# Optimization experiments

Measured on AMD Instinct MI355X. Metric: run time of the kernel, lower is better.

## Reference

```python
import jax, jax.numpy as jnp
import numpy as np

B, IN_UNITS, IN_CHANNELS, NUM_UNITS, UNIT_SIZE = 128, 32, 4096, 10, 16
NUM_ITER = 3


def setup_inputs() -> dict:
    key = jax.random.key(0)
    k1, k2 = jax.random.split(key)
    # x: primary-capsule output [B, in_units, in_channels]
    x = jax.random.normal(k1, (B, IN_UNITS, IN_CHANNELS), dtype=jnp.float32)
    # W: routing weights, torch param shape [1, C, J, D, K] with batch dim dropped
    W = jax.random.normal(k2, (IN_CHANNELS, NUM_UNITS, UNIT_SIZE, IN_UNITS), dtype=jnp.float32)
    return {"x": x, "W": W}


def reference(x, W):
    b_sz = x.shape[0]
    C, J = W.shape[0], W.shape[1]
    # torch: x.transpose(1,2) -> [B,C,K]; u_hat = W @ x -> [B,C,J,D,1]
    # u_hat[b,i,j,d] = sum_k W[i,j,d,k] * x[b,k,i]
    u_hat = jnp.einsum('ijdk,bki->bijd', W, x)  # [B, C, J, D]
    b_ij = jnp.zeros((C, J), dtype=x.dtype)
    v = None
    for _ in range(NUM_ITER):
        # faithful: softmax over dim=1 (in_channels axis), not over classes
        c_ij = jax.nn.softmax(b_ij, axis=0)               # [C, J]
        s = jnp.einsum('ij,bijd->bjd', c_ij, u_hat)        # [B, J, D]
        # faithful squash: original sums over dim=2 of [B,1,J,D,1] == class axis J
        mag_sq = jnp.sum(s * s, axis=1, keepdims=True)     # [B, 1, D]
        v = (mag_sq / (1.0 + mag_sq)) * (s / jnp.sqrt(mag_sq))
        # agreement: <u_hat, v> averaged over batch
        agree = jnp.einsum('bijd,bjd->ij', u_hat, v) / b_sz
        b_ij = b_ij + agree
    # torch returns v_j.squeeze(1): [B, J, D, 1]
    return v[:, :, :, None]
```

## Files before the change

### kernel.cpp

```cpp
#include <hip/hip_runtime.h>


typedef __attribute__((ext_vector_type(8))) __bf16 bf16x8;
typedef __attribute__((ext_vector_type(4))) float  f32x4;
typedef __attribute__((ext_vector_type(8))) unsigned short u16x8;
typedef __attribute__((ext_vector_type(4))) unsigned int  u32x4;

#define DI __device__ __forceinline__

DI float bf2f(unsigned short u){ unsigned int x = ((unsigned int)u) << 16; return __builtin_bit_cast(float, x); }
DI unsigned short f2bf(float f){
  unsigned int u = __builtin_bit_cast(unsigned int, f);
  u += 0x7fffu + ((u >> 16) & 1u);
  return (unsigned short)(u >> 16);
}
DI unsigned int cvtpk(float lo, float hi){
  unsigned int r;
  asm("v_cvt_pk_bf16_f32 %0, %1, %2" : "=v"(r) : "v"(lo), "v"(hi));
  return r;
}

constexpr int Ci = 4096, Kk = 32, Jj = 10, Dd = 16, Bb = 128;
constexpr int KI = Ci * Kk;
constexpr int JDt = Jj * Dd;
constexpr int NCH = 256, CK = 512;

constexpr size_t OFF_W2 = 0;
constexpr size_t SZ_W2  = (size_t)JDt * KI * 2;
constexpr size_t OFF_XT = OFF_W2 + SZ_W2;
constexpr size_t SZ_XT  = (size_t)KI * Bb * 2;
constexpr size_t OFF_XB = OFF_XT + SZ_XT;
constexpr size_t SZ_XB  = (size_t)Bb * KI * 2;
constexpr size_t OFF_BT = OFF_XB + SZ_XB;
constexpr size_t SZ_BT  = (size_t)Jj * Ci * 4;
constexpr size_t OFF_CT = OFF_BT + SZ_BT;
constexpr size_t OFF_VBT = OFF_CT + SZ_BT;
constexpr size_t SZ_VBT = (size_t)JDt * Bb * 2;
constexpr size_t OFF_SP = OFF_VBT + SZ_VBT;
constexpr size_t SZ_SP  = (size_t)NCH * Bb * JDt * 4;

constexpr int WPAD = 522;
__global__ __launch_bounds__(512) void pack_w(const float* __restrict__ W, unsigned short* __restrict__ w2){
  __shared__ unsigned short t16[64 * WPAD];
  const int mt = blockIdx.x % 10, it = blockIdx.x / 10;
  const int m0 = mt * 512, i0 = it * 64;
  #pragma unroll
  for(int u=0; u<16; u++){
    int e = threadIdx.x + 512*u;
    int row = e >> 7, c4 = e & 127;
    float4 v = *(const float4*)(W + (size_t)(i0+row)*5120 + m0 + c4*4);
    unsigned int* p = (unsigned int*)(t16 + row*WPAD + c4*4);
    p[0] = cvtpk(v.x, v.y);
    p[1] = cvtpk(v.z, v.w);
  }
  __syncthreads();
  #pragma unroll
  for(int u=0; u<8; u++){
    int e = threadIdx.x + 512*u;
    int mr = e >> 3, g = e & 7;
    u32x4 o;
    #pragma unroll
    for(int j=0; j<4; j++){
      unsigned int lo = t16[(g*8 + 2*j    )*WPAD + mr];
      unsigned int hi = t16[(g*8 + 2*j + 1)*WPAD + mr];
      o[j] = lo | (hi << 16);
    }
    *(u32x4*)(w2 + (size_t)(m0+mr)*Ci + i0 + g*8) = o;
  }
}

constexpr int XPAD = 134;
__global__ __launch_bounds__(256) void pack_xt(const float* __restrict__ x, unsigned short* __restrict__ xT,
                                               unsigned short* __restrict__ xbf, float* __restrict__ bT){
  __shared__ float tile[64 * XPAD];
  const int bid = blockIdx.x;
  if(bid >= 2048){
    ((f32x4*)bT)[(bid-2048)*256 + threadIdx.x] = f32x4{0.f,0.f,0.f,0.f};
    return;
  }
  const int ki0 = (bid >> 1) * 128, b0 = (bid & 1) * 64;
  #pragma unroll
  for(int u=0; u<8; u++){
    int e = threadIdx.x + 256*u;
    int row = e >> 5, q = e & 31;
    float4 v = *(const float4*)(x + (size_t)(b0+row)*KI + ki0 + q*4);
    float2* p = (float2*)(tile + row*XPAD + q*4);
    p[0] = float2{v.x, v.y};
    p[1] = float2{v.z, v.w};
  }
  __syncthreads();
  #pragma unroll
  for(int u=0; u<4; u++){
    int e = threadIdx.x + 256*u;
    int kir = e >> 3, g = e & 7;
    u32x4 o;
    #pragma unroll
    for(int j=0; j<4; j++)
      o[j] = cvtpk(tile[(g*8 + 2*j)*XPAD + kir], tile[(g*8 + 2*j + 1)*XPAD + kir]);
    *(u32x4*)(xT + (size_t)(ki0+kir)*Bb + b0 + g*8) = o;
  }
  #pragma unroll
  for(int u=0; u<4; u++){
    int e = threadIdx.x + 256*u;
    int row = e >> 4, sg = e & 15;
    u32x4 o;
    #pragma unroll
    for(int j=0; j<4; j++)
      o[j] = cvtpk(tile[row*XPAD + sg*8 + 2*j], tile[row*XPAD + sg*8 + 2*j + 1]);
    *(u32x4*)(xbf + (size_t)(b0+row)*KI + ki0 + sg*8) = o;
  }
}

__global__ __launch_bounds__(256) void softmax_k(const float* __restrict__ bT, float* __restrict__ cT){
  const int j = blockIdx.x, tid = threadIdx.x, lane = tid & 63, wid = tid >> 6;
  __shared__ float red[4];
  float vals[16];
  float mx = -3.4e38f;
  #pragma unroll
  for(int u=0; u<16; u++){ vals[u] = bT[j*Ci + tid + 256*u]; mx = fmaxf(mx, vals[u]); }
  #pragma unroll
  for(int o=32; o>0; o>>=1) mx = fmaxf(mx, __shfl_xor(mx, o));
  if(lane == 0) red[wid] = mx;
  __syncthreads();
  mx = fmaxf(fmaxf(red[0],red[1]), fmaxf(red[2],red[3]));
  float sm = 0.f;
  #pragma unroll
  for(int u=0; u<16; u++){ vals[u] = expf(vals[u]-mx); sm += vals[u]; }
  #pragma unroll
  for(int o=32; o>0; o>>=1) sm += __shfl_xor(sm, o);
  __syncthreads();
  if(lane == 0) red[wid] = sm;
  __syncthreads();
  sm = red[0]+red[1]+red[2]+red[3];
  float inv = 1.0f / sm;
  #pragma unroll
  for(int u=0; u<16; u++) cT[j*Ci + tid + 256*u] = vals[u]*inv;
}

__global__ __launch_bounds__(512) void s_pass(const unsigned short* __restrict__ xbf,
                                              const unsigned short* __restrict__ w2,
                                              const float* __restrict__ cT,
                                              float* __restrict__ spart){
  __shared__ unsigned short xs[2][128*64];
  __shared__ unsigned short wsm[2][160*64];
  const int tid = threadIdx.x, lane = tid & 63, wid = tid >> 6;
  const int wb = wid & 3, wj = wid >> 2;
  const int ki0 = blockIdx.x * CK;
  const float cu = 1.0f/4096.0f;

  const int xb_ = tid >> 3, xsg = tid & 7;
  f32x4 acc[2][5];
  #pragma unroll
  for(int m=0;m<2;m++)
    #pragma unroll
    for(int n=0;n<5;n++) acc[m][n] = f32x4{0.f,0.f,0.f,0.f};

  u16x8 xv0, xv1; u16x8 wv[3]; int ibn;

  #define S_LOAD(STEP) { \
    const int kb = ki0 + (STEP)*64; \
    xv0 = *(const u16x8*)(xbf + (size_t)xb_*KI + kb + xsg*8); \
    xv1 = *(const u16x8*)(xbf + (size_t)(xb_+64)*KI + kb + xsg*8); \
    ibn = kb & (Ci-1); \
    _Pragma("unroll") \
    for(int u=0; u<3; u++){ int e = tid + 512*u; if(e < 1280){ \
      int jd = e>>3, sg = e&7; \
      wv[u] = *(const u16x8*)(w2 + (size_t)jd*KI + kb + sg*8); \
    }} }

  #define S_WRITE(BUF) { \
    *(u16x8*)((char*)xs[BUF] + xb_*128 + ((xsg*16) ^ ((xb_&7)<<4))) = xv0; \
    *(u16x8*)((char*)xs[BUF] + (xb_+64)*128 + ((xsg*16) ^ ((xb_&7)<<4))) = xv1; \
    _Pragma("unroll") \
    for(int u=0; u<3; u++){ int e = tid + 512*u; if(e < 1280){ \
      int jd = e>>3, sg = e&7; \
      float f[8]; \
      _Pragma("unroll") \
      for(int q=0;q<8;q++) f[q] = bf2f(wv[u][q]); \
      if(cT){ \
        const float* cp = cT + (jd>>4)*Ci + ibn + sg*8; \
        float4 c0 = *(const float4*)cp; float4 c1 = *(const float4*)(cp+4); \
        f[0]*=c0.x; f[1]*=c0.y; f[2]*=c0.z; f[3]*=c0.w; \
        f[4]*=c1.x; f[5]*=c1.y; f[6]*=c1.z; f[7]*=c1.w; \
      } else { \
        _Pragma("unroll") \
        for(int q=0;q<8;q++) f[q] *= cu; \
      } \
      u32x4 wo; \
      wo[0]=cvtpk(f[0],f[1]); wo[1]=cvtpk(f[2],f[3]); \
      wo[2]=cvtpk(f[4],f[5]); wo[3]=cvtpk(f[6],f[7]); \
      *(u32x4*)((char*)wsm[BUF] + jd*128 + ((sg*16) ^ ((jd&7)<<4))) = wo; \
    }} }

  S_LOAD(0); S_WRITE(0);
  __syncthreads();
  int cur = 0;
  for(int step=0; step<8; ++step){
    if(step < 7) S_LOAD(step+1);
    #pragma unroll
    for(int ks=0; ks<2; ks++){
      const int kk2 = (ks*32 + ((lane>>4)<<3)) * 2;
      bf16x8 a[2];
      #pragma unroll
      for(int m=0;m<2;m++){
        int row = wb*32 + m*16 + (lane&15);
        a[m] = *(const bf16x8*)((const char*)xs[cur] + row*128 + (kk2 ^ ((row&7)<<4)));
      }
      #pragma unroll
      for(int n=0;n<5;n++){
        int row = wj*80 + n*16 + (lane&15);
        bf16x8 bb = *(const bf16x8*)((const char*)wsm[cur] + row*128 + (kk2 ^ ((row&7)<<4)));
        acc[0][n] = __builtin_amdgcn_mfma_f32_16x16x32_bf16(a[0], bb, acc[0][n], 0,0,0);
        acc[1][n] = __builtin_amdgcn_mfma_f32_16x16x32_bf16(a[1], bb, acc[1][n], 0,0,0);
      }
    }
    if(step < 7) S_WRITE(cur^1);
    __syncthreads();
    cur ^= 1;
  }
  float* sp = spart + (size_t)blockIdx.x * (Bb*JDt);
  #pragma unroll
  for(int m=0;m<2;m++)
    #pragma unroll
    for(int n=0;n<5;n++)
      #pragma unroll
      for(int r=0;r<4;r++){
        int b  = wb*32 + m*16 + ((lane>>4)<<2) + r;
        int jd = wj*80 + n*16 + (lane&15);
        sp[b*JDt + jd] = acc[m][n][r];
      }
}

__global__ __launch_bounds__(256) void redsq(const float* __restrict__ spart,
                                             float* __restrict__ vout,
                                             unsigned short* __restrict__ vbT){
  const int b = blockIdx.x, tid = threadIdx.x;
  __shared__ float sred[6][JDt];
  __shared__ float sq[JDt];
  __shared__ float scale[Dd];
  float s = 0.f;
  if(tid < 240){
    const int g = tid % 40, cg = tid / 40;
    f32x4 a = {0.f,0.f,0.f,0.f};
    for(int ch=cg; ch<NCH; ch+=6)
      a += *(const f32x4*)(spart + (size_t)ch*(Bb*JDt) + b*JDt + g*4);
    *(f32x4*)&sred[cg][g*4] = a;
  }
  __syncthreads();
  if(tid < JDt){
    #pragma unroll
    for(int c=0;c<6;c++) s += sred[c][tid];
    sq[tid] = s*s;
  }
  __syncthreads();
  if(tid < Dd){
    float m = 0.f;
    #pragma unroll
    for(int j=0;j<Jj;j++) m += sq[j*Dd + tid];
    scale[tid] = sqrtf(m) / (1.0f + m);
  }
  __syncthreads();
  if(tid < JDt){
    float v = s * scale[tid & (Dd-1)];
    vout[b*JDt + tid] = v;
    vbT[tid*Bb + b] = f2bf(v);
  }
}

__global__ __launch_bounds__(256) void agree_pass(const unsigned short* __restrict__ xT,
                                                  const unsigned short* __restrict__ vbT,
                                                  const unsigned short* __restrict__ w2,
                                                  float* __restrict__ bT){
  const int tid = threadIdx.x, lane = tid & 63, wid = tid >> 6;
  const int wj = wid & 1, wk = wid >> 1;
  const int ki0 = blockIdx.x * 64;
  const int bsl = (lane>>4)<<3;
  f32x4 acc[5][2];
  #pragma unroll
  for(int m=0;m<5;m++){ acc[m][0]=f32x4{0,0,0,0}; acc[m][1]=f32x4{0,0,0,0}; }
  #pragma unroll
  for(int ks=0; ks<4; ks++){
    bf16x8 af[5];
    #pragma unroll
    for(int m=0;m<5;m++){
      int jd = wj*80 + m*16 + (lane&15);
      af[m] = *(const bf16x8*)(vbT + jd*Bb + ks*32 + bsl);
    }
    #pragma unroll
    for(int n=0;n<2;n++){
      int kir = ki0 + wk*32 + n*16 + (lane&15);
      bf16x8 bf_ = *(const bf16x8*)(xT + (size_t)kir*Bb + ks*32 + bsl);
      #pragma unroll
      for(int m=0;m<5;m++)
        acc[m][n] = __builtin_amdgcn_mfma_f32_16x16x32_bf16(af[m], bf_, acc[m][n], 0,0,0);
    }
  }
  const int ibase = ki0 & (Ci-1);
  #pragma unroll
  for(int m=0;m<5;m++){
    int j = wj*5 + m;
    #pragma unroll
    for(int n=0;n<2;n++){
      int colg = ki0 + wk*32 + n*16 + (lane&15);
      float s = 0.f;
      #pragma unroll
      for(int r=0;r<4;r++){
        int jdrow = wj*80 + m*16 + ((lane>>4)<<2) + r;
        s += acc[m][n][r] * bf2f(w2[(size_t)jdrow*KI + colg]);
      }
      s += __shfl_xor(s, 16);
      s += __shfl_xor(s, 32);
      if(lane < 16){
        int ig = ibase + wk*32 + n*16 + lane;
        atomicAdd(bT + j*Ci + ig, s * (1.0f/128.0f));
      }
    }
  }
}

extern "C" void kernel_launch(void* const* d_in, const int* in_sizes, int n_in,
                              void* d_out, int out_size, void* d_ws, size_t ws_size,
                              hipStream_t stream) {
  const float* x = (const float*)d_in[0];
  const float* W = (const float*)d_in[1];
  float* out = (float*)d_out;
  char* ws = (char*)d_ws;
  unsigned short* w2  = (unsigned short*)(ws + OFF_W2);
  unsigned short* xT  = (unsigned short*)(ws + OFF_XT);
  unsigned short* xbf = (unsigned short*)(ws + OFF_XB);
  float* bT           = (float*)(ws + OFF_BT);
  float* cT           = (float*)(ws + OFF_CT);
  unsigned short* vbT = (unsigned short*)(ws + OFF_VBT);
  float* spart        = (float*)(ws + OFF_SP);

  pack_w<<<640, 512, 0, stream>>>(W, w2);
  pack_xt<<<2088, 256, 0, stream>>>(x, xT, xbf, bT);
  for(int t=0; t<3; t++){
    if(t > 0) softmax_k<<<Jj, 256, 0, stream>>>(bT, cT);
    s_pass<<<NCH, 512, 0, stream>>>(xbf, w2, (t==0)? nullptr : cT, spart);
    redsq<<<Bb, 256, 0, stream>>>(spart, out, vbT);
    if(t < 2) agree_pass<<<KI/64, 256, 0, stream>>>(xT, vbT, w2, bT);
  }
}
```

Baseline: 240.3 us.

## Fuse routing iterations into one cooperative persistent kernel with grid syncs

Replaces the per-iteration chain of softmax, s_pass, redsq and agree_pass launches with a single cooperative kernel of 256 blocks that runs all three routing iterations, separating the phases with grid-wide syncs. The agree phase is remapped so each 512-thread block covers eight 64-column slices instead of 2048 small blocks. This removes about ten kernel launches and their gaps. In exchange it adds grid barriers, leaves most blocks idle during the softmax and squash phases, and reduces parallelism in the agree phase.

Result: slower. 584.7 us (+143.3%).

```diff
diff --git a/kernel.cpp b/kernel.cpp
--- a/kernel.cpp
+++ b/kernel.cpp
@@ -1,4 +1,7 @@
 #include <hip/hip_runtime.h>
+#include <hip/hip_cooperative_groups.h>
+
+namespace cg = cooperative_groups;
 
 
 typedef __attribute__((ext_vector_type(8))) __bf16 bf16x8;
@@ -9,15 +12,15 @@
 #define DI __device__ __forceinline__
 
 DI float bf2f(unsigned short u){ unsigned int x = ((unsigned int)u) << 16; return __builtin_bit_cast(float, x); }
+DI unsigned int cvtpk(float lo, float hi){
+  unsigned int r;
+  asm("v_cvt_pk_bf16_f32 %0, %1, %2" : "=v"(r) : "v"(lo), "v"(hi));
+  return r;
+}
 DI unsigned short f2bf(float f){
   unsigned int u = __builtin_bit_cast(unsigned int, f);
   u += 0x7fffu + ((u >> 16) & 1u);
   return (unsigned short)(u >> 16);
-}
-DI unsigned int cvtpk(float lo, float hi){
-  unsigned int r;
-  asm("v_cvt_pk_bf16_f32 %0, %1, %2" : "=v"(r) : "v"(lo), "v"(hi));
-  return r;
 }
 
 constexpr int Ci = 4096, Kk = 32, Jj = 10, Dd = 16, Bb = 128;
@@ -111,211 +114,230 @@
   }
 }
 
-__global__ __launch_bounds__(256) void softmax_k(const float* __restrict__ bT, float* __restrict__ cT){
-  const int j = blockIdx.x, tid = threadIdx.x, lane = tid & 63, wid = tid >> 6;
-  __shared__ float red[4];
-  float vals[16];
-  float mx = -3.4e38f;
-  #pragma unroll
-  for(int u=0; u<16; u++){ vals[u] = bT[j*Ci + tid + 256*u]; mx = fmaxf(mx, vals[u]); }
-  #pragma unroll
-  for(int o=32; o>0; o>>=1) mx = fmaxf(mx, __shfl_xor(mx, o));
-  if(lane == 0) red[wid] = mx;
-  __syncthreads();
-  mx = fmaxf(fmaxf(red[0],red[1]), fmaxf(red[2],red[3]));
-  float sm = 0.f;
-  #pragma unroll
-  for(int u=0; u<16; u++){ vals[u] = expf(vals[u]-mx); sm += vals[u]; }
-  #pragma unroll
-  for(int o=32; o>0; o>>=1) sm += __shfl_xor(sm, o);
-  __syncthreads();
-  if(lane == 0) red[wid] = sm;
-  __syncthreads();
-  sm = red[0]+red[1]+red[2]+red[3];
-  float inv = 1.0f / sm;
-  #pragma unroll
-  for(int u=0; u<16; u++) cT[j*Ci + tid + 256*u] = vals[u]*inv;
-}
-
-__global__ __launch_bounds__(512) void s_pass(const unsigned short* __restrict__ xbf,
-                                              const unsigned short* __restrict__ w2,
-                                              const float* __restrict__ cT,
-                                              float* __restrict__ spart){
-  __shared__ unsigned short xs[2][128*64];
-  __shared__ unsigned short wsm[2][160*64];
+__global__ __launch_bounds__(512) void routing(const unsigned short* __restrict__ xbf,
+                                               const unsigned short* __restrict__ xT,
+                                               const unsigned short* __restrict__ w2,
+                                               float* __restrict__ bT,
+                                               float* __restrict__ cT,
+                                               unsigned short* __restrict__ vbT,
+                                               float* __restrict__ spart,
+                                               float* __restrict__ vout){
+  cg::grid_group grid = cg::this_grid();
+  __shared__ __align__(16) char smem[73728];
   const int tid = threadIdx.x, lane = tid & 63, wid = tid >> 6;
-  const int wb = wid & 3, wj = wid >> 2;
-  const int ki0 = blockIdx.x * CK;
   const float cu = 1.0f/4096.0f;
 
-  const int xb_ = tid >> 3, xsg = tid & 7;
-  f32x4 acc[2][5];
-  #pragma unroll
-  for(int m=0;m<2;m++)
-    #pragma unroll
-    for(int n=0;n<5;n++) acc[m][n] = f32x4{0.f,0.f,0.f,0.f};
-
-  u16x8 xv0, xv1; u16x8 wv[3]; int ibn;
-
-  #define S_LOAD(STEP) { \
-    const int kb = ki0 + (STEP)*64; \
-    xv0 = *(const u16x8*)(xbf + (size_t)xb_*KI + kb + xsg*8); \
-    xv1 = *(const u16x8*)(xbf + (size_t)(xb_+64)*KI + kb + xsg*8); \
-    ibn = kb & (Ci-1); \
-    _Pragma("unroll") \
-    for(int u=0; u<3; u++){ int e = tid + 512*u; if(e < 1280){ \
-      int jd = e>>3, sg = e&7; \
-      wv[u] = *(const u16x8*)(w2 + (size_t)jd*KI + kb + sg*8); \
-    }} }
-
-  #define S_WRITE(BUF) { \
-    *(u16x8*)((char*)xs[BUF] + xb_*128 + ((xsg*16) ^ ((xb_&7)<<4))) = xv0; \
-    *(u16x8*)((char*)xs[BUF] + (xb_+64)*128 + ((xsg*16) ^ ((xb_&7)<<4))) = xv1; \
-    _Pragma("unroll") \
-    for(int u=0; u<3; u++){ int e = tid + 512*u; if(e < 1280){ \
-      int jd = e>>3, sg = e&7; \
-      float f[8]; \
-      _Pragma("unroll") \
-      for(int q=0;q<8;q++) f[q] = bf2f(wv[u][q]); \
-      if(cT){ \
-        const float* cp = cT + (jd>>4)*Ci + ibn + sg*8; \
-        float4 c0 = *(const float4*)cp; float4 c1 = *(const float4*)(cp+4); \
-        f[0]*=c0.x; f[1]*=c0.y; f[2]*=c0.z; f[3]*=c0.w; \
-        f[4]*=c1.x; f[5]*=c1.y; f[6]*=c1.z; f[7]*=c1.w; \
-      } else { \
+  #define XSP(BUF) ((char*)smem + (BUF)*16384)
+  #define WSP(BUF) ((char*)smem + 32768 + (BUF)*20480)
+
+  for(int t=0; t<3; ++t){
+    if(t > 0){
+      if(blockIdx.x < Jj){
+        const int j = blockIdx.x;
+        float* redm = (float*)smem;
+        float* reds = (float*)smem + 8;
+        float vals[8]; float mx = -3.4e38f;
+        #pragma unroll
+        for(int u=0; u<8; u++){ vals[u] = bT[j*Ci + tid + 512*u]; mx = fmaxf(mx, vals[u]); }
+        #pragma unroll
+        for(int o=32; o>0; o>>=1) mx = fmaxf(mx, __shfl_xor(mx, o));
+        if(lane == 0) redm[wid] = mx;
+        __syncthreads();
+        mx = fmaxf(fmaxf(fmaxf(redm[0],redm[1]),fmaxf(redm[2],redm[3])),
+                   fmaxf(fmaxf(redm[4],redm[5]),fmaxf(redm[6],redm[7])));
+        float sm = 0.f;
+        #pragma unroll
+        for(int u=0; u<8; u++){ vals[u] = expf(vals[u]-mx); sm += vals[u]; }
+        #pragma unroll
+        for(int o=32; o>0; o>>=1) sm += __shfl_xor(sm, o);
+        if(lane == 0) reds[wid] = sm;
+        __syncthreads();
+        sm = reds[0]+reds[1]+reds[2]+reds[3]+reds[4]+reds[5]+reds[6]+reds[7];
+        float inv = 1.0f / sm;
+        #pragma unroll
+        for(int u=0; u<8; u++) cT[j*Ci + tid + 512*u] = vals[u]*inv;
+      }
+      grid.sync();
+    }
+
+    {
+      const bool useC = (t > 0);
+      const int wb = wid & 3, wj = wid >> 2;
+      const int ki0 = blockIdx.x * CK;
+      const int xb_ = tid >> 3, xsg = tid & 7;
+      f32x4 acc[2][5];
+      #pragma unroll
+      for(int m=0;m<2;m++)
+        #pragma unroll
+        for(int n=0;n<5;n++) acc[m][n] = f32x4{0.f,0.f,0.f,0.f};
+
+      u16x8 xv0, xv1; u16x8 wv[3]; int ibn;
+
+      #define S_LOAD(STEP) { \
+        const int kb = ki0 + (STEP)*64; \
+        xv0 = *(const u16x8*)(xbf + (size_t)xb_*KI + kb + xsg*8); \
+        xv1 = *(const u16x8*)(xbf + (size_t)(xb_+64)*KI + kb + xsg*8); \
+        ibn = kb & (Ci-1); \
         _Pragma("unroll") \
-        for(int q=0;q<8;q++) f[q] *= cu; \
-      } \
-      u32x4 wo; \
-      wo[0]=cvtpk(f[0],f[1]); wo[1]=cvtpk(f[2],f[3]); \
-      wo[2]=cvtpk(f[4],f[5]); wo[3]=cvtpk(f[6],f[7]); \
-      *(u32x4*)((char*)wsm[BUF] + jd*128 + ((sg*16) ^ ((jd&7)<<4))) = wo; \
-    }} }
-
-  S_LOAD(0); S_WRITE(0);
-  __syncthreads();
-  int cur = 0;
-  for(int step=0; step<8; ++step){
-    if(step < 7) S_LOAD(step+1);
-    #pragma unroll
-    for(int ks=0; ks<2; ks++){
-      const int kk2 = (ks*32 + ((lane>>4)<<3)) * 2;
-      bf16x8 a[2];
+        for(int u=0; u<3; u++){ int e = tid + 512*u; if(e < 1280){ \
+          int jd = e>>3, sg = e&7; \
+          wv[u] = *(const u16x8*)(w2 + (size_t)jd*KI + kb + sg*8); \
+        }} }
+
+      #define S_WRITE(BUF) { \
+        *(u16x8*)(XSP(BUF) + xb_*128 + ((xsg*16) ^ ((xb_&7)<<4))) = xv0; \
+        *(u16x8*)(XSP(BUF) + (xb_+64)*128 + ((xsg*16) ^ ((xb_&7)<<4))) = xv1; \
+        _Pragma("unroll") \
+        for(int u=0; u<3; u++){ int e = tid + 512*u; if(e < 1280){ \
+          int jd = e>>3, sg = e&7; \
+          float f[8]; \
+          _Pragma("unroll") \
+          for(int q=0;q<8;q++) f[q] = bf2f(wv[u][q]); \
+          if(useC){ \
+            const float* cp = cT + (jd>>4)*Ci + ibn + sg*8; \
+            float4 c0 = *(const float4*)cp; float4 c1 = *(const float4*)(cp+4); \
+            f[0]*=c0.x; f[1]*=c0.y; f[2]*=c0.z; f[3]*=c0.w; \
+            f[4]*=c1.x; f[5]*=c1.y; f[6]*=c1.z; f[7]*=c1.w; \
+          } else { \
+            _Pragma("unroll") \
+            for(int q=0;q<8;q++) f[q] *= cu; \
+          } \
+          u32x4 wo; \
+          wo[0]=cvtpk(f[0],f[1]); wo[1]=cvtpk(f[2],f[3]); \
+          wo[2]=cvtpk(f[4],f[5]); wo[3]=cvtpk(f[6],f[7]); \
+          *(u32x4*)(WSP(BUF) + jd*128 + ((sg*16) ^ ((jd&7)<<4))) = wo; \
+        }} }
+
+      S_LOAD(0); S_WRITE(0);
+      __syncthreads();
+      int cur = 0;
+      for(int step=0; step<8; ++step){
+        if(step < 7) S_LOAD(step+1);
+        #pragma unroll
+        for(int ks=0; ks<2; ks++){
+          const int kk2 = (ks*32 + ((lane>>4)<<3)) * 2;
+          bf16x8 a[2];
+          #pragma unroll
+          for(int m=0;m<2;m++){
+            int row = wb*32 + m*16 + (lane&15);
+            a[m] = *(const bf16x8*)(XSP(cur) + row*128 + (kk2 ^ ((row&7)<<4)));
+          }
+          #pragma unroll
+          for(int n=0;n<5;n++){
+            int row = wj*80 + n*16 + (lane&15);
+            bf16x8 bb = *(const bf16x8*)(WSP(cur) + row*128 + (kk2 ^ ((row&7)<<4)));
+            acc[0][n] = __builtin_amdgcn_mfma_f32_16x16x32_bf16(a[0], bb, acc[0][n], 0,0,0);
+            acc[1][n] = __builtin_amdgcn_mfma_f32_16x16x32_bf16(a[1], bb, acc[1][n], 0,0,0);
+          }
+        }
+        if(step < 7) S_WRITE(cur^1);
+        __syncthreads();
+        cur ^= 1;
+      }
+      float* sp = spart + (size_t)blockIdx.x * (Bb*JDt);
       #pragma unroll
-      for(int m=0;m<2;m++){
-        int row = wb*32 + m*16 + (lane&15);
-        a[m] = *(const bf16x8*)((const char*)xs[cur] + row*128 + (kk2 ^ ((row&7)<<4)));
-      }
-      #pragma unroll
-      for(int n=0;n<5;n++){
-        int row = wj*80 + n*16 + (lane&15);
-        bf16x8 bb = *(const bf16x8*)((const char*)wsm[cur] + row*128 + (kk2 ^ ((row&7)<<4)));
-        acc[0][n] = __builtin_amdgcn_mfma_f32_16x16x32_bf16(a[0], bb, acc[0][n], 0,0,0);
-        acc[1][n] = __builtin_amdgcn_mfma_f32_16x16x32_bf16(a[1], bb, acc[1][n], 0,0,0);
-      }
-    }
-    if(step < 7) S_WRITE(cur^1);
-    __syncthreads();
-    cur ^= 1;
-  }
-  float* sp = spart + (size_t)blockIdx.x * (Bb*JDt);
-  #pragma unroll
-  for(int m=0;m<2;m++)
-    #pragma unroll
-    for(int n=0;n<5;n++)
-      #pragma unroll
-      for(int r=0;r<4;r++){
-        int b  = wb*32 + m*16 + ((lane>>4)<<2) + r;
-        int jd = wj*80 + n*16 + (lane&15);
-        sp[b*JDt + jd] = acc[m][n][r];
-      }
-}
-
-__global__ __launch_bounds__(256) void redsq(const float* __restrict__ spart,
-                                             float* __restrict__ vout,
-                                             unsigned short* __restrict__ vbT){
-  const int b = blockIdx.x, tid = threadIdx.x;
-  __shared__ float sred[6][JDt];
-  __shared__ float sq[JDt];
-  __shared__ float scale[Dd];
-  float s = 0.f;
-  if(tid < 240){
-    const int g = tid % 40, cg = tid / 40;
-    f32x4 a = {0.f,0.f,0.f,0.f};
-    for(int ch=cg; ch<NCH; ch+=6)
-      a += *(const f32x4*)(spart + (size_t)ch*(Bb*JDt) + b*JDt + g*4);
-    *(f32x4*)&sred[cg][g*4] = a;
-  }
-  __syncthreads();
-  if(tid < JDt){
-    #pragma unroll
-    for(int c=0;c<6;c++) s += sred[c][tid];
-    sq[tid] = s*s;
-  }
-  __syncthreads();
-  if(tid < Dd){
-    float m = 0.f;
-    #pragma unroll
-    for(int j=0;j<Jj;j++) m += sq[j*Dd + tid];
-    scale[tid] = sqrtf(m) / (1.0f + m);
-  }
-  __syncthreads();
-  if(tid < JDt){
-    float v = s * scale[tid & (Dd-1)];
-    vout[b*JDt + tid] = v;
-    vbT[tid*Bb + b] = f2bf(v);
-  }
-}
-
-__global__ __launch_bounds__(256) void agree_pass(const unsigned short* __restrict__ xT,
-                                                  const unsigned short* __restrict__ vbT,
-                                                  const unsigned short* __restrict__ w2,
-                                                  float* __restrict__ bT){
-  const int tid = threadIdx.x, lane = tid & 63, wid = tid >> 6;
-  const int wj = wid & 1, wk = wid >> 1;
-  const int ki0 = blockIdx.x * 64;
-  const int bsl = (lane>>4)<<3;
-  f32x4 acc[5][2];
-  #pragma unroll
-  for(int m=0;m<5;m++){ acc[m][0]=f32x4{0,0,0,0}; acc[m][1]=f32x4{0,0,0,0}; }
-  #pragma unroll
-  for(int ks=0; ks<4; ks++){
-    bf16x8 af[5];
-    #pragma unroll
-    for(int m=0;m<5;m++){
-      int jd = wj*80 + m*16 + (lane&15);
-      af[m] = *(const bf16x8*)(vbT + jd*Bb + ks*32 + bsl);
-    }
-    #pragma unroll
-    for(int n=0;n<2;n++){
-      int kir = ki0 + wk*32 + n*16 + (lane&15);
-      bf16x8 bf_ = *(const bf16x8*)(xT + (size_t)kir*Bb + ks*32 + bsl);
-      #pragma unroll
-      for(int m=0;m<5;m++)
-        acc[m][n] = __builtin_amdgcn_mfma_f32_16x16x32_bf16(af[m], bf_, acc[m][n], 0,0,0);
-    }
-  }
-  const int ibase = ki0 & (Ci-1);
-  #pragma unroll
-  for(int m=0;m<5;m++){
-    int j = wj*5 + m;
-    #pragma unroll
-    for(int n=0;n<2;n++){
-      int colg = ki0 + wk*32 + n*16 + (lane&15);
+      for(int m=0;m<2;m++)
+        #pragma unroll
+        for(int n=0;n<5;n++)
+          #pragma unroll
+          for(int r=0;r<4;r++){
+            int b  = wb*32 + m*16 + ((lane>>4)<<2) + r;
+            int jd = wj*80 + n*16 + (lane&15);
+            sp[b*JDt + jd] = acc[m][n][r];
+          }
+    }
+    grid.sync();
+
+    if(blockIdx.x < Bb){
+      const int b = blockIdx.x;
+      float* sred = (float*)smem;
+      float* sq   = (float*)smem + 6*JDt;
+      float* scal = (float*)smem + 7*JDt;
       float s = 0.f;
-      #pragma unroll
-      for(int r=0;r<4;r++){
-        int jdrow = wj*80 + m*16 + ((lane>>4)<<2) + r;
-        s += acc[m][n][r] * bf2f(w2[(size_t)jdrow*KI + colg]);
-      }
-      s += __shfl_xor(s, 16);
-      s += __shfl_xor(s, 32);
-      if(lane < 16){
-        int ig = ibase + wk*32 + n*16 + lane;
-        atomicAdd(bT + j*Ci + ig, s * (1.0f/128.0f));
-      }
-    }
-  }
+      if(tid < 240){
+        const int g = tid % 40, cg2 = tid / 40;
+        f32x4 a = {0.f,0.f,0.f,0.f};
+        for(int ch=cg2; ch<NCH; ch+=6)
+          a += *(const f32x4*)(spart + (size_t)ch*(Bb*JDt) + b*JDt + g*4);
+        *(f32x4*)&sred[cg2*JDt + g*4] = a;
+      }
+      __syncthreads();
+      if(tid < JDt){
+        #pragma unroll
+        for(int c=0;c<6;c++) s += sred[c*JDt + tid];
+        sq[tid] = s*s;
+      }
+      __syncthreads();
+      if(tid < Dd){
+        float m = 0.f;
+        #pragma unroll
+        for(int j=0;j<Jj;j++) m += sq[j*Dd + tid];
+        scal[tid] = sqrtf(m) / (1.0f + m);
+      }
+      __syncthreads();
+      if(tid < JDt){
+        float v = s * scal[tid & (Dd-1)];
+        vout[b*JDt + tid] = v;
+        vbT[tid*Bb + b] = f2bf(v);
+      }
+    }
+    grid.sync();
+
+    if(t < 2){
+      const int p = wid >> 2, wq = wid & 3;
+      const int wj = wq & 1, wk = wq >> 1;
+      const int bsl = (lane>>4)<<3;
+      for(int si=0; si<4; ++si){
+        const int ki0 = (blockIdx.x*8 + si*2 + p) * 64;
+        f32x4 acc[5][2];
+        #pragma unroll
+        for(int m=0;m<5;m++){ acc[m][0]=f32x4{0,0,0,0}; acc[m][1]=f32x4{0,0,0,0}; }
+        #pragma unroll
+        for(int ks=0; ks<4; ks++){
+          bf16x8 af[5];
+          #pragma unroll
+          for(int m=0;m<5;m++){
+            int jd = wj*80 + m*16 + (lane&15);
+            af[m] = *(const bf16x8*)(vbT + jd*Bb + ks*32 + bsl);
+          }
+          #pragma unroll
+          for(int n=0;n<2;n++){
+            int kir = ki0 + wk*32 + n*16 + (lane&15);
+            bf16x8 bf_ = *(const bf16x8*)(xT + (size_t)kir*Bb + ks*32 + bsl);
+            #pragma unroll
+            for(int m=0;m<5;m++)
+              acc[m][n] = __builtin_amdgcn_mfma_f32_16x16x32_bf16(af[m], bf_, acc[m][n], 0,0,0);
+          }
+        }
+        const int ibase = ki0 & (Ci-1);
+        #pragma unroll
+        for(int m=0;m<5;m++){
+          int j = wj*5 + m;
+          #pragma unroll
+          for(int n=0;n<2;n++){
+            int colg = ki0 + wk*32 + n*16 + (lane&15);
+            float s2 = 0.f;
+            #pragma unroll
+            for(int r=0;r<4;r++){
+              int jdrow = wj*80 + m*16 + ((lane>>4)<<2) + r;
+              s2 += acc[m][n][r] * bf2f(w2[(size_t)jdrow*KI + colg]);
+            }
+            s2 += __shfl_xor(s2, 16);
+            s2 += __shfl_xor(s2, 32);
+            if(lane < 16){
+              int ig = ibase + wk*32 + n*16 + lane;
+              atomicAdd(bT + j*Ci + ig, s2 * (1.0f/128.0f));
+            }
+          }
+        }
+      }
+      grid.sync();
+    }
+  }
+  #undef S_LOAD
+  #undef S_WRITE
+  #undef XSP
+  #undef WSP
 }
 
 extern "C" void kernel_launch(void* const* d_in, const int* in_sizes, int n_in,
@@ -325,20 +347,18 @@
   const float* W = (const float*)d_in[1];
   float* out = (float*)d_out;
   char* ws = (char*)d_ws;
-  unsigned short* w2  = (unsigned short*)(ws + OFF_W2);
-  unsigned short* xT  = (unsigned short*)(ws + OFF_XT);
-  unsigned short* xbf = (unsigned short*)(ws + OFF_XB);
+  const unsigned short* w2  = (const unsigned short*)(ws + OFF_W2);
+  const unsigned short* xT  = (const unsigned short*)(ws + OFF_XT);
+  const unsigned short* xbf = (const unsigned short*)(ws + OFF_XB);
   float* bT           = (float*)(ws + OFF_BT);
   float* cT           = (float*)(ws + OFF_CT);
   unsigned short* vbT = (unsigned short*)(ws + OFF_VBT);
   float* spart        = (float*)(ws + OFF_SP);
 
-  pack_w<<<640, 512, 0, stream>>>(W, w2);
-  pack_xt<<<2088, 256, 0, stream>>>(x, xT, xbf, bT);
-  for(int t=0; t<3; t++){
-    if(t > 0) softmax_k<<<Jj, 256, 0, stream>>>(bT, cT);
-    s_pass<<<NCH, 512, 0, stream>>>(xbf, w2, (t==0)? nullptr : cT, spart);
-    redsq<<<Bb, 256, 0, stream>>>(spart, out, vbT);
-    if(t < 2) agree_pass<<<KI/64, 256, 0, stream>>>(xT, vbT, w2, bT);
-  }
-}
+  pack_w<<<640, 512, 0, stream>>>(W, (unsigned short*)w2);
+  pack_xt<<<2088, 256, 0, stream>>>(x, (unsigned short*)xT, (unsigned short*)xbf, bT);
+
+  void* args[] = { (void*)&xbf, (void*)&xT, (void*)&w2, (void*)&bT,
+                   (void*)&cT, (void*)&vbT, (void*)&spart, (void*)&out };
+  hipLaunchCooperativeKernel((const void*)routing, dim3(NCH), dim3(512), args, 0, stream);
+}
```
